# Performance work log

Hardware: AMD Instinct MI355X
Metric: run time of the kernel (lower is better)

## Reference

```python
import jax, jax.numpy as jnp
import numpy as np

S, D = 4096, 512


def setup_inputs() -> dict:
    key = jax.random.key(0)
    ks = jax.random.split(key, 10)
    names = ['x', 'w_ql', 'w_kl', 'w_qr', 'w_kr', 'w_qg', 'w_kg', 'w_qloc', 'w_kloc', 'w_v']
    shapes = [(S, D)] + [(D, D)] * 9
    scale = [1.0] + [float(np.sqrt(2.0 / (D + D)))] * 9  # xavier-ish for weights
    return {n: jax.random.normal(k, sh, dtype=jnp.float32) * s
            for n, k, sh, s in zip(names, ks, shapes, scale)}


def reference(x, w_ql, w_kl, w_qr, w_kr, w_qg, w_kg, w_qloc, w_kloc, w_v):
    # x: [S, D]
    s, d = x.shape
    norm = jnp.sqrt(jnp.asarray(d, x.dtype))
    # strict upper triangle (j > i) is masked for the left boundary,
    # strict lower triangle (i > j) for the right boundary
    mask_up = jnp.triu(jnp.ones((s, s), dtype=bool), k=1)

    ql, kl = x @ w_ql, x @ w_kl
    qr, kr = x @ w_qr, x @ w_kr

    neg_inf = jnp.asarray(-jnp.inf, x.dtype)
    left_scores = jnp.where(mask_up, neg_inf, ql @ kl.T) / norm            # [S,S]
    left_boundary = jax.nn.softmax(left_scores, axis=1)
    right_scores = jnp.where(mask_up.T, neg_inf, qr @ kr.T) / norm
    right_boundary = jax.nn.softmax(right_scores, axis=1)

    # left_boundary @ triu(ones)  == forward cumsum along columns
    # right_boundary @ tril(ones) == reverse cumsum along columns
    left_cdf = jnp.cumsum(left_boundary, axis=1)
    right_cdf = jnp.cumsum(right_boundary[:, ::-1], axis=1)[:, ::-1]
    att_mask = left_cdf * right_cdf                                        # [S,S]

    s_glb = (x @ w_qg) @ (x @ w_kg).T                                      # [S,S]
    s_loc = ((x @ w_qloc) @ (x @ w_kloc).T) * att_mask                     # additive local path
    score = (s_glb + s_loc) / norm

    att_weight = jax.nn.softmax(score, axis=1)
    att_output = att_weight @ (x @ w_v)                                    # [S,D]
    return att_output, att_weight
```

## Files before the change

### kernel.cpp

```cpp
#include <hip/hip_runtime.h>


#define SS 4096
#define DD 512
#define INV_NORM 0.04419417382415922f

typedef _Float16 f16;
typedef f16 f16x8 __attribute__((ext_vector_type(8)));
typedef f16 f16x4 __attribute__((ext_vector_type(4)));
typedef float f32x4 __attribute__((ext_vector_type(4)));
typedef unsigned short ushort;
typedef ushort ushort4v __attribute__((ext_vector_type(4)));

#define GAS __attribute__((address_space(1)))
#define LAS __attribute__((address_space(3)))

__device__ __forceinline__ void ldsdma16(const void* g, void* l) {
  __builtin_amdgcn_global_load_lds((const GAS void*)g, (LAS void*)l, 16, 0, 0);
}

__device__ __forceinline__ ushort f2bf(float f) {
  unsigned u = __float_as_uint(f);
  return (ushort)((u + 0x7FFFu + ((u >> 16) & 1u)) >> 16);
}
__device__ __forceinline__ float bf2f(ushort h) {
  return __uint_as_float((unsigned)h << 16);
}

__device__ __forceinline__ void stage16(const f16* __restrict__ src, int ldk, f16* lds, int k0) {
  const int tid  = threadIdx.x;
  const int lane = tid & 63;
  const int wv   = tid >> 6;
  const int rb   = wv * 8 + (lane >> 3);
  const int cs   = lane & 7;
#pragma unroll
  for (int c = 0; c < 4; ++c) {
    const int r = c * 32 + rb;
    const int q = cs ^ (r & 7);
    ldsdma16(src + (size_t)r * ldk + k0 + q * 8, lds + c * 2048 + wv * 512);
  }
}

__device__ __forceinline__ f16x8 fragld(const f16* lds, int r0, int qb) {
  const int lane = threadIdx.x & 63;
  const int r = r0 + (lane & 15);
  const int q = (qb + (lane >> 4)) ^ (r & 7);
  return *(const f16x8*)(lds + r * 64 + q * 8);
}

__device__ __forceinline__ void mma64(const f16* As, const f16* Bs, f32x4 acc[2][8]) {
  const int wv = threadIdx.x >> 6;
#pragma unroll
  for (int ks = 0; ks < 2; ++ks) {
    const f16x8 a0 = fragld(As, wv * 32,      ks * 4);
    const f16x8 a1 = fragld(As, wv * 32 + 16, ks * 4);
#pragma unroll
    for (int j = 0; j < 8; ++j) {
      const f16x8 b = fragld(Bs, j * 16, ks * 4);
      acc[0][j] = __builtin_amdgcn_mfma_f32_16x16x32_f16(a0, b, acc[0][j], 0, 0, 0);
      acc[1][j] = __builtin_amdgcn_mfma_f32_16x16x32_f16(a1, b, acc[1][j], 0, 0, 0);
    }
  }
}

__global__ void k_cvt_x(const float* __restrict__ x, f16* __restrict__ xh) {
  const size_t i = ((size_t)blockIdx.x * 256 + threadIdx.x) * 4;
  const float4 f = *(const float4*)(x + i);
  f16x4 h = { (f16)f.x, (f16)f.y, (f16)f.z, (f16)f.w };
  *(f16x4*)(xh + i) = h;
}

__global__ void k_trw(const float* w0, const float* w1, const float* w2, const float* w3,
                      const float* w4, const float* w5, const float* w6, const float* w7,
                      const float* w8, f16* __restrict__ wt) {
  const float* srcs[9] = {w0, w1, w2, w3, w4, w5, w6, w7, w8};
  const float* src = srcs[blockIdx.z];
  f16* dst = wt + (size_t)blockIdx.z * DD * DD;
  __shared__ float t[32][33];
  const int n0 = blockIdx.x * 32, k0 = blockIdx.y * 32;
  const int tx = threadIdx.x, ty = threadIdx.y;
#pragma unroll
  for (int i = 0; i < 32; i += 8)
    t[ty + i][tx] = src[(size_t)(k0 + ty + i) * DD + n0 + tx];
  __syncthreads();
#pragma unroll
  for (int i = 0; i < 32; i += 8)
    dst[(size_t)(n0 + ty + i) * DD + k0 + tx] = (f16)t[tx][ty + i];
}

__global__ void k_trv(const f16* __restrict__ v, f16* __restrict__ vt) {
  __shared__ f16 t[32][33];
  const int n0 = blockIdx.x * 32, s0 = blockIdx.y * 32;
  const int tx = threadIdx.x, ty = threadIdx.y;
#pragma unroll
  for (int i = 0; i < 32; i += 8)
    t[ty + i][tx] = v[(size_t)(s0 + ty + i) * DD + n0 + tx];
  __syncthreads();
#pragma unroll
  for (int i = 0; i < 32; i += 8)
    vt[(size_t)(n0 + ty + i) * SS + s0 + tx] = t[tx][ty + i];
}

__global__ __launch_bounds__(256, 3) void k_proj(const f16* __restrict__ xh,
                                                 const f16* __restrict__ wt,
                                                 f16* __restrict__ proj) {
  __shared__ __align__(16) f16 As[8192];
  __shared__ __align__(16) f16 Bs[8192];
  const int z = blockIdx.z;
  const f16* B = wt + (size_t)z * DD * DD;
  f16* C = proj + (size_t)z * SS * DD;
  const int R0 = blockIdx.y * 128, C0 = blockIdx.x * 128;
  f32x4 acc[2][8];
#pragma unroll
  for (int i = 0; i < 2; ++i)
#pragma unroll
    for (int j = 0; j < 8; ++j) acc[i][j] = (f32x4){0.f, 0.f, 0.f, 0.f};
  for (int kb = 0; kb < DD / 64; ++kb) {
    __syncthreads();
    stage16(xh + (size_t)R0 * DD, DD, As, kb * 64);
    stage16(B  + (size_t)C0 * DD, DD, Bs, kb * 64);
    __syncthreads();
    mma64(As, Bs, acc);
  }
  const int lane = threadIdx.x & 63, wv = threadIdx.x >> 6;
  const int mm = lane & 15, quad = lane >> 4;
#pragma unroll
  for (int i = 0; i < 2; ++i)
#pragma unroll
    for (int j = 0; j < 8; ++j)
#pragma unroll
      for (int r = 0; r < 4; ++r)
        C[(size_t)(R0 + wv * 32 + i * 16 + quad * 4 + r) * DD + C0 + j * 16 + mm] =
            (f16)acc[i][j][r];
}

__global__ __launch_bounds__(256, 3) void k_bnd(const f16* __restrict__ proj,
                                                f16* __restrict__ eL,
                                                f16* __restrict__ eR) {
  const int t = blockIdx.x, dir = blockIdx.y;
  int rbk = (int)((sqrtf(8.f * t + 1.f) - 1.f) * 0.5f);
  while ((rbk + 1) * (rbk + 2) / 2 <= t) ++rbk;
  while (rbk * (rbk + 1) / 2 > t) --rbk;
  int jt = t - rbk * (rbk + 1) / 2;
  if (dir) { jt = 31 - jt; rbk = 31 - rbk; }
  __shared__ __align__(16) f16 As[8192];
  __shared__ __align__(16) f16 Bs[8192];
  const f16* q  = proj + (size_t)(dir ? 2 : 0) * SS * DD;
  const f16* kp = proj + (size_t)(dir ? 3 : 1) * SS * DD;
  const int R0 = rbk * 128, C0 = jt * 128;
  f32x4 acc[2][8];
#pragma unroll
  for (int i = 0; i < 2; ++i)
#pragma unroll
    for (int j = 0; j < 8; ++j) acc[i][j] = (f32x4){0.f, 0.f, 0.f, 0.f};
  for (int kb = 0; kb < DD / 64; ++kb) {
    __syncthreads();
    stage16(q  + (size_t)R0 * DD, DD, As, kb * 64);
    stage16(kp + (size_t)C0 * DD, DD, Bs, kb * 64);
    __syncthreads();
    mma64(As, Bs, acc);
  }
  const int lane = threadIdx.x & 63, wv = threadIdx.x >> 6;
  const int mm = lane & 15, quad = lane >> 4;
  const bool diag = (jt == rbk);
  f16* outp = dir ? eR : eL;
#pragma unroll
  for (int i = 0; i < 2; ++i)
#pragma unroll
    for (int r = 0; r < 4; ++r) {
      const int rl = wv * 32 + i * 16 + quad * 4 + r;
#pragma unroll
      for (int j = 0; j < 8; ++j) {
        const int cl = j * 16 + mm;
        const float sc = acc[i][j][r] * INV_NORM;
        const bool bad = diag && (dir ? (cl < rl) : (cl > rl));
        const float e = bad ? 0.f : __expf(sc);
        outp[(size_t)(R0 + rl) * SS + (C0 + cl)] = (f16)e;
      }
    }
}

__global__ __launch_bounds__(1024) void k_cumsum(f16* __restrict__ eL,
                                                 const f16* __restrict__ eR) {
  const int i = blockIdx.x;
  const int tid = threadIdx.x, lane = tid & 63, wv = tid >> 6;
  __shared__ float wsL[16], wsR[16];
  const int j0 = tid * 4;

  float pl[4] = {0.f, 0.f, 0.f, 0.f};
  if (j0 <= i) {
    const f16x4 hl = *(const f16x4*)(eL + (size_t)i * SS + j0);
#pragma unroll
    for (int u = 0; u < 4; ++u) pl[u] = (j0 + u <= i) ? (float)hl[u] : 0.f;
  }
#pragma unroll
  for (int u = 1; u < 4; ++u) pl[u] += pl[u - 1];
  const float Tl = pl[3];
  float sl = Tl;
#pragma unroll
  for (int d = 1; d < 64; d <<= 1) {
    const float o = __shfl_up(sl, (unsigned)d, 64);
    if (lane >= d) sl += o;
  }
  if (lane == 63) wsL[wv] = sl;

  float rr[4] = {0.f, 0.f, 0.f, 0.f}, pr[4];
  if (j0 + 3 >= i) {
    const f16x4 hr = *(const f16x4*)(eR + (size_t)i * SS + j0);
#pragma unroll
    for (int u = 0; u < 4; ++u) rr[u] = (j0 + u >= i) ? (float)hr[u] : 0.f;
  }
  pr[0] = rr[0];
#pragma unroll
  for (int u = 1; u < 4; ++u) pr[u] = pr[u - 1] + rr[u];
  const float Tr = pr[3];
  float sr = Tr;
#pragma unroll
  for (int d = 1; d < 64; d <<= 1) {
    const float o = __shfl_up(sr, (unsigned)d, 64);
    if (lane >= d) sr += o;
  }
  if (lane == 63) wsR[wv] = sr;

  __syncthreads();
  float offL = 0.f, totL = 0.f, offR = 0.f, totR = 0.f;
#pragma unroll
  for (int ww = 0; ww < 16; ++ww) {
    const float a = wsL[ww], b = wsR[ww];
    if (ww < wv) { offL += a; offR += b; }
    totL += a; totR += b;
  }
  const float exL = offL + sl - Tl;
  const float exR = offR + sr - Tr;
  const float invL = 1.f / totL, invR = 1.f / totR;

  f16x4 out;
#pragma unroll
  for (int u = 0; u < 4; ++u) {
    const int j = j0 + u;
    const float cdfL = (exL + pl[u]) * invL;
    const float pre  = exR + pr[u];
    const float cdfR = (totR - pre + rr[u]) * invR;
    const float m = (j < i) ? cdfL : ((j > i) ? cdfR : 1.f);
    out[u] = (f16)m;
  }
  *(f16x4*)(eL + (size_t)i * SS + j0) = out;
}

__global__ __launch_bounds__(256, 2) void k_score(const f16* __restrict__ proj,
                                                  const f16* __restrict__ mask,
                                                  f16* __restrict__ ehalf,
                                                  float* __restrict__ lsc) {
  __shared__ __align__(16) f16 Ag[8192];
  __shared__ __align__(16) f16 Bg[8192];
  __shared__ __align__(16) f16 Al[8192];
  __shared__ __align__(16) f16 Bl[8192];
  const int jt = blockIdx.x, rbk = blockIdx.y;
  const f16* qg = proj + (size_t)4 * SS * DD;
  const f16* kg = proj + (size_t)5 * SS * DD;
  const f16* ql = proj + (size_t)6 * SS * DD;
  const f16* kl = proj + (size_t)7 * SS * DD;
  const int R0 = rbk * 128, C0 = jt * 128;
  f32x4 ag[2][8], al[2][8];
#pragma unroll
  for (int i = 0; i < 2; ++i)
#pragma unroll
    for (int j = 0; j < 8; ++j) {
      ag[i][j] = (f32x4){0.f, 0.f, 0.f, 0.f};
      al[i][j] = (f32x4){0.f, 0.f, 0.f, 0.f};
    }
  for (int kb = 0; kb < DD / 64; ++kb) {
    __syncthreads();
    stage16(qg + (size_t)R0 * DD, DD, Ag, kb * 64);
    stage16(kg + (size_t)C0 * DD, DD, Bg, kb * 64);
    stage16(ql + (size_t)R0 * DD, DD, Al, kb * 64);
    stage16(kl + (size_t)C0 * DD, DD, Bl, kb * 64);
    __syncthreads();
    mma64(Ag, Bg, ag);
    mma64(Al, Bl, al);
  }
  const int lane = threadIdx.x & 63, wv = threadIdx.x >> 6;
  const int mm = lane & 15, quad = lane >> 4;
  float ls[2][4];
#pragma unroll
  for (int i = 0; i < 2; ++i)
#pragma unroll
    for (int r = 0; r < 4; ++r) ls[i][r] = 0.f;
#pragma unroll
  for (int i = 0; i < 2; ++i)
#pragma unroll
    for (int r = 0; r < 4; ++r) {
      const int rg = R0 + wv * 32 + i * 16 + quad * 4 + r;
#pragma unroll
      for (int j = 0; j < 8; ++j) {
        const int cg = C0 + j * 16 + mm;
        const float mk = (float)mask[(size_t)rg * SS + cg];
        const float scv = (ag[i][j][r] + al[i][j][r] * mk) * INV_NORM;
        const float e = __expf(scv);
        ehalf[(size_t)rg * SS + cg] = (f16)e;
        ls[i][r] += e;
      }
    }
#pragma unroll
  for (int d = 1; d < 16; d <<= 1)
#pragma unroll
    for (int i = 0; i < 2; ++i)
#pragma unroll
      for (int r = 0; r < 4; ++r)
        ls[i][r] += __shfl_xor(ls[i][r], d, 64);
  if (mm == 0) {
#pragma unroll
    for (int i = 0; i < 2; ++i)
#pragma unroll
      for (int r = 0; r < 4; ++r)
        atomicAdd(&lsc[R0 + wv * 32 + i * 16 + quad * 4 + r], ls[i][r]);
  }
}

__global__ __launch_bounds__(256, 4) void k_pv(const f16* __restrict__ ehalf,
                                               const f16* __restrict__ vt,
                                               ushort* __restrict__ part) {
  __shared__ __align__(16) f16 As[8192];
  __shared__ __align__(16) f16 Bs[8192];
  const int C0 = blockIdx.x * 128, R0 = blockIdx.y * 128, zk = blockIdx.z;
  f32x4 acc[2][8];
#pragma unroll
  for (int i = 0; i < 2; ++i)
#pragma unroll
    for (int j = 0; j < 8; ++j) acc[i][j] = (f32x4){0.f, 0.f, 0.f, 0.f};
  for (int kb = 0; kb < 16; ++kb) {
    const int k0 = zk * 1024 + kb * 64;
    __syncthreads();
    stage16(ehalf + (size_t)R0 * SS, SS, As, k0);
    stage16(vt    + (size_t)C0 * SS, SS, Bs, k0);
    __syncthreads();
    mma64(As, Bs, acc);
  }
  const int lane = threadIdx.x & 63, wv = threadIdx.x >> 6;
  const int mm = lane & 15, quad = lane >> 4;
  ushort* P = part + (size_t)zk * SS * DD;
#pragma unroll
  for (int i = 0; i < 2; ++i)
#pragma unroll
    for (int j = 0; j < 8; ++j)
#pragma unroll
      for (int r = 0; r < 4; ++r)
        P[(size_t)(R0 + wv * 32 + i * 16 + quad * 4 + r) * DD + C0 + j * 16 + mm] =
            f2bf(acc[i][j][r]);
}

__global__ void k_fin(const f16* __restrict__ ehalf, const ushort* __restrict__ part,
                      const float* __restrict__ lsc, float* __restrict__ outw,
                      float* __restrict__ O) {
  const int bx = blockIdx.x;
  if (bx < 8192) {
    const size_t idx = ((size_t)bx * 256 + threadIdx.x) * 8;
    const int row = (int)(idx >> 12);
    const float inv = 1.f / lsc[row];
    const f16x8 h = *(const f16x8*)(ehalf + idx);
    float4 a = { (float)h[0] * inv, (float)h[1] * inv, (float)h[2] * inv, (float)h[3] * inv };
    float4 b = { (float)h[4] * inv, (float)h[5] * inv, (float)h[6] * inv, (float)h[7] * inv };
    *(float4*)(outw + idx) = a;
    *(float4*)(outw + idx + 4) = b;
  } else {
    const size_t idx = ((size_t)(bx - 8192) * 256 + threadIdx.x) * 4;
    const int row = (int)(idx >> 9);
    float s0 = 0.f, s1 = 0.f, s2 = 0.f, s3 = 0.f;
#pragma unroll
    for (int p = 0; p < 4; ++p) {
      const ushort4v v = *(const ushort4v*)(part + (size_t)p * SS * DD + idx);
      s0 += bf2f(v[0]); s1 += bf2f(v[1]); s2 += bf2f(v[2]); s3 += bf2f(v[3]);
    }
    const float inv = 1.f / lsc[row];
    float4 s = { s0 * inv, s1 * inv, s2 * inv, s3 * inv };
    *(float4*)(O + idx) = s;
  }
}

extern "C" void kernel_launch(void* const* d_in, const int* in_sizes, int n_in,
                              void* d_out, int out_size, void* d_ws, size_t ws_size,
                              hipStream_t stream) {
  (void)in_sizes; (void)n_in; (void)out_size; (void)ws_size;
  const float* x = (const float*)d_in[0];
  const float* w[9];
  for (int i = 0; i < 9; ++i) w[i] = (const float*)d_in[1 + i];
  float* O    = (float*)d_out;
  float* outw = O + (size_t)SS * DD;

  char* ws = (char*)d_ws;
  size_t off = 0;
  auto alloc = [&](size_t b) { void* p = ws + off; off += (b + 255) & ~(size_t)255; return p; };
  f16* xh     = (f16*)alloc((size_t)SS * DD * 2);
  f16* wt     = (f16*)alloc((size_t)9 * DD * DD * 2);
  f16* proj   = (f16*)alloc((size_t)9 * SS * DD * 2);
  f16* vt     = (f16*)alloc((size_t)DD * SS * 2);
  f16* eL     = (f16*)alloc((size_t)SS * SS * 2);
  f16* eR     = (f16*)alloc((size_t)SS * SS * 2);
  f16* ehalf  = (f16*)alloc((size_t)SS * SS * 2);
  float* lsc  = (float*)alloc((size_t)SS * 4);
  ushort* part = (ushort*)eR;

  hipMemsetAsync(lsc, 0, (size_t)SS * 4, stream);
  k_cvt_x<<<SS * DD / 1024, 256, 0, stream>>>(x, xh);
  k_trw<<<dim3(16, 16, 9), dim3(32, 8), 0, stream>>>(w[0], w[1], w[2], w[3], w[4],
                                                     w[5], w[6], w[7], w[8], wt);
  k_proj<<<dim3(4, 32, 9), 256, 0, stream>>>(xh, wt, proj);
  k_trv<<<dim3(16, 128), dim3(32, 8), 0, stream>>>(proj + (size_t)8 * SS * DD, vt);
  k_bnd<<<dim3(528, 2), 256, 0, stream>>>(proj, eL, eR);
  k_cumsum<<<SS, 1024, 0, stream>>>(eL, eR);
  k_score<<<dim3(32, 32), 256, 0, stream>>>(proj, eL, ehalf, lsc);
  k_pv<<<dim3(4, 32, 4), 256, 0, stream>>>(ehalf, vt, part);
  k_fin<<<10240, 256, 0, stream>>>(ehalf, part, lsc, outw, O);
}
```

Measured before the change: 293.3 us.

## Stage GEMM epilogues through swizzled LDS for coalesced 16-byte stores; fuse small launches

The output tiles of the projection, boundary, score and PV GEMMs are first written into an XOR-swizzled LDS buffer. Each block then writes them to global memory as coalesced 16-byte vectors, replacing scattered 2-byte stores. The score kernel also loads its mask tile into LDS with vector loads. The x conversion is folded into the weight-transpose launch, and the lsc memset moves into k_cumsum, which removes two launches. The cost is extra barriers and LDS traffic in every epilogue.

```diff
diff --git a/kernel.cpp b/kernel.cpp
--- a/kernel.cpp
+++ b/kernel.cpp
@@ -10,7 +10,6 @@
 typedef f16 f16x4 __attribute__((ext_vector_type(4)));
 typedef float f32x4 __attribute__((ext_vector_type(4)));
 typedef unsigned short ushort;
-typedef ushort ushort4v __attribute__((ext_vector_type(4)));
 
 #define GAS __attribute__((address_space(1)))
 #define LAS __attribute__((address_space(3)))
@@ -25,6 +24,10 @@
 }
 __device__ __forceinline__ float bf2f(ushort h) {
   return __uint_as_float((unsigned)h << 16);
+}
+
+__device__ __forceinline__ int eswz(int r, int c) {
+  return r * 128 + (c ^ (((r >> 2) & 3) << 4));
 }
 
 __device__ __forceinline__ void stage16(const f16* __restrict__ src, int ldk, f16* lds, int k0) {
@@ -63,19 +66,37 @@
   }
 }
 
-__global__ void k_cvt_x(const float* __restrict__ x, f16* __restrict__ xh) {
-  const size_t i = ((size_t)blockIdx.x * 256 + threadIdx.x) * 4;
-  const float4 f = *(const float4*)(x + i);
-  f16x4 h = { (f16)f.x, (f16)f.y, (f16)f.z, (f16)f.w };
-  *(f16x4*)(xh + i) = h;
+__device__ __forceinline__ void tile_out(const f16* T, f16* __restrict__ dst,
+                                         int R0, int C0, int ld) {
+#pragma unroll
+  for (int it = 0; it < 8; ++it) {
+    const int o = it * 256 + threadIdx.x;
+    const int rr = o >> 4, c8 = (o & 15) * 8;
+    const f16x8 v = *(const f16x8*)&T[eswz(rr, c8)];
+    *(f16x8*)(dst + (size_t)(R0 + rr) * ld + C0 + c8) = v;
+  }
 }
 
 __global__ void k_trw(const float* w0, const float* w1, const float* w2, const float* w3,
                       const float* w4, const float* w5, const float* w6, const float* w7,
-                      const float* w8, f16* __restrict__ wt) {
+                      const float* w8, const float* __restrict__ x,
+                      f16* __restrict__ wt, f16* __restrict__ xh) {
+  const int z = blockIdx.z;
+  if (z == 9) {
+    const int b = blockIdx.y * 16 + blockIdx.x;
+    const int t = b * 256 + (threadIdx.y * 32 + threadIdx.x);
+    const size_t base = (size_t)t * 32;
+#pragma unroll
+    for (int u = 0; u < 8; ++u) {
+      const float4 f = *(const float4*)(x + base + u * 4);
+      f16x4 h = { (f16)f.x, (f16)f.y, (f16)f.z, (f16)f.w };
+      *(f16x4*)(xh + base + u * 4) = h;
+    }
+    return;
+  }
   const float* srcs[9] = {w0, w1, w2, w3, w4, w5, w6, w7, w8};
-  const float* src = srcs[blockIdx.z];
-  f16* dst = wt + (size_t)blockIdx.z * DD * DD;
+  const float* src = srcs[z];
+  f16* dst = wt + (size_t)z * DD * DD;
   __shared__ float t[32][33];
   const int n0 = blockIdx.x * 32, k0 = blockIdx.y * 32;
   const int tx = threadIdx.x, ty = threadIdx.y;
@@ -104,8 +125,9 @@
 __global__ __launch_bounds__(256, 3) void k_proj(const f16* __restrict__ xh,
                                                  const f16* __restrict__ wt,
                                                  f16* __restrict__ proj) {
-  __shared__ __align__(16) f16 As[8192];
-  __shared__ __align__(16) f16 Bs[8192];
+  __shared__ __align__(16) f16 SH[16384];
+  f16* As = SH;
+  f16* Bs = SH + 8192;
   const int z = blockIdx.z;
   const f16* B = wt + (size_t)z * DD * DD;
   f16* C = proj + (size_t)z * SS * DD;
@@ -124,14 +146,16 @@
   }
   const int lane = threadIdx.x & 63, wv = threadIdx.x >> 6;
   const int mm = lane & 15, quad = lane >> 4;
+  __syncthreads();
 #pragma unroll
   for (int i = 0; i < 2; ++i)
 #pragma unroll
     for (int j = 0; j < 8; ++j)
 #pragma unroll
       for (int r = 0; r < 4; ++r)
-        C[(size_t)(R0 + wv * 32 + i * 16 + quad * 4 + r) * DD + C0 + j * 16 + mm] =
-            (f16)acc[i][j][r];
+        SH[eswz(wv * 32 + i * 16 + quad * 4 + r, j * 16 + mm)] = (f16)acc[i][j][r];
+  __syncthreads();
+  tile_out(SH, C, R0, C0, DD);
 }
 
 __global__ __launch_bounds__(256, 3) void k_bnd(const f16* __restrict__ proj,
@@ -143,8 +167,9 @@
   while (rbk * (rbk + 1) / 2 > t) --rbk;
   int jt = t - rbk * (rbk + 1) / 2;
   if (dir) { jt = 31 - jt; rbk = 31 - rbk; }
-  __shared__ __align__(16) f16 As[8192];
-  __shared__ __align__(16) f16 Bs[8192];
+  __shared__ __align__(16) f16 SH[16384];
+  f16* As = SH;
+  f16* Bs = SH + 8192;
   const f16* q  = proj + (size_t)(dir ? 2 : 0) * SS * DD;
   const f16* kp = proj + (size_t)(dir ? 3 : 1) * SS * DD;
   const int R0 = rbk * 128, C0 = jt * 128;
@@ -163,7 +188,7 @@
   const int lane = threadIdx.x & 63, wv = threadIdx.x >> 6;
   const int mm = lane & 15, quad = lane >> 4;
   const bool diag = (jt == rbk);
-  f16* outp = dir ? eR : eL;
+  __syncthreads();
 #pragma unroll
   for (int i = 0; i < 2; ++i)
 #pragma unroll
@@ -174,17 +199,20 @@
         const int cl = j * 16 + mm;
         const float sc = acc[i][j][r] * INV_NORM;
         const bool bad = diag && (dir ? (cl < rl) : (cl > rl));
-        const float e = bad ? 0.f : __expf(sc);
-        outp[(size_t)(R0 + rl) * SS + (C0 + cl)] = (f16)e;
+        SH[eswz(rl, cl)] = (f16)(bad ? 0.f : __expf(sc));
       }
     }
+  __syncthreads();
+  tile_out(SH, dir ? eR : eL, R0, C0, SS);
 }
 
 __global__ __launch_bounds__(1024) void k_cumsum(f16* __restrict__ eL,
-                                                 const f16* __restrict__ eR) {
+                                                 const f16* __restrict__ eR,
+                                                 float* __restrict__ lsc) {
   const int i = blockIdx.x;
   const int tid = threadIdx.x, lane = tid & 63, wv = tid >> 6;
   __shared__ float wsL[16], wsR[16];
+  if (tid == 0) lsc[i] = 0.f;
   const int j0 = tid * 4;
 
   float pl[4] = {0.f, 0.f, 0.f, 0.f};
@@ -251,10 +279,11 @@
                                                   const f16* __restrict__ mask,
                                                   f16* __restrict__ ehalf,
                                                   float* __restrict__ lsc) {
-  __shared__ __align__(16) f16 Ag[8192];
-  __shared__ __align__(16) f16 Bg[8192];
-  __shared__ __align__(16) f16 Al[8192];
-  __shared__ __align__(16) f16 Bl[8192];
+  __shared__ __align__(16) f16 SH[32768];
+  f16* Ag = SH;
+  f16* Bg = SH + 8192;
+  f16* Al = SH + 16384;
+  f16* Bl = SH + 24576;
   const int jt = blockIdx.x, rbk = blockIdx.y;
   const f16* qg = proj + (size_t)4 * SS * DD;
   const f16* kg = proj + (size_t)5 * SS * DD;
@@ -281,6 +310,16 @@
   }
   const int lane = threadIdx.x & 63, wv = threadIdx.x >> 6;
   const int mm = lane & 15, quad = lane >> 4;
+  __syncthreads();
+#pragma unroll
+  for (int it = 0; it < 8; ++it) {
+    const int o = it * 256 + threadIdx.x;
+    const int rr = o >> 4, c8 = (o & 15) * 8;
+    const f16x8 m = *(const f16x8*)(mask + (size_t)(R0 + rr) * SS + C0 + c8);
+    *(f16x8*)&SH[eswz(rr, c8)] = m;
+  }
+  __syncthreads();
+  f16* TE = SH + 16384;
   float ls[2][4];
 #pragma unroll
   for (int i = 0; i < 2; ++i)
@@ -290,14 +329,14 @@
   for (int i = 0; i < 2; ++i)
 #pragma unroll
     for (int r = 0; r < 4; ++r) {
-      const int rg = R0 + wv * 32 + i * 16 + quad * 4 + r;
+      const int rl = wv * 32 + i * 16 + quad * 4 + r;
 #pragma unroll
       for (int j = 0; j < 8; ++j) {
-        const int cg = C0 + j * 16 + mm;
-        const float mk = (float)mask[(size_t)rg * SS + cg];
+        const int cl = j * 16 + mm;
+        const float mk = (float)SH[eswz(rl, cl)];
         const float scv = (ag[i][j][r] + al[i][j][r] * mk) * INV_NORM;
         const float e = __expf(scv);
-        ehalf[(size_t)rg * SS + cg] = (f16)e;
+        TE[eswz(rl, cl)] = (f16)e;
         ls[i][r] += e;
       }
     }
@@ -315,13 +354,16 @@
       for (int r = 0; r < 4; ++r)
         atomicAdd(&lsc[R0 + wv * 32 + i * 16 + quad * 4 + r], ls[i][r]);
   }
+  __syncthreads();
+  tile_out(TE, ehalf, R0, C0, SS);
 }
 
 __global__ __launch_bounds__(256, 4) void k_pv(const f16* __restrict__ ehalf,
                                                const f16* __restrict__ vt,
                                                ushort* __restrict__ part) {
-  __shared__ __align__(16) f16 As[8192];
-  __shared__ __align__(16) f16 Bs[8192];
+  __shared__ __align__(16) f16 SH[16384];
+  f16* As = SH;
+  f16* Bs = SH + 8192;
   const int C0 = blockIdx.x * 128, R0 = blockIdx.y * 128, zk = blockIdx.z;
   f32x4 acc[2][8];
 #pragma unroll
@@ -338,15 +380,17 @@
   }
   const int lane = threadIdx.x & 63, wv = threadIdx.x >> 6;
   const int mm = lane & 15, quad = lane >> 4;
-  ushort* P = part + (size_t)zk * SS * DD;
+  ushort* TU = (ushort*)SH;
+  __syncthreads();
 #pragma unroll
   for (int i = 0; i < 2; ++i)
 #pragma unroll
     for (int j = 0; j < 8; ++j)
 #pragma unroll
       for (int r = 0; r < 4; ++r)
-        P[(size_t)(R0 + wv * 32 + i * 16 + quad * 4 + r) * DD + C0 + j * 16 + mm] =
-            f2bf(acc[i][j][r]);
+        TU[eswz(wv * 32 + i * 16 + quad * 4 + r, j * 16 + mm)] = f2bf(acc[i][j][r]);
+  __syncthreads();
+  tile_out(SH, (f16*)(part + (size_t)zk * SS * DD), R0, C0, DD);
 }
 
 __global__ void k_fin(const f16* __restrict__ ehalf, const ushort* __restrict__ part,
@@ -366,6 +410,7 @@
     const size_t idx = ((size_t)(bx - 8192) * 256 + threadIdx.x) * 4;
     const int row = (int)(idx >> 9);
     float s0 = 0.f, s1 = 0.f, s2 = 0.f, s3 = 0.f;
+    typedef ushort ushort4v __attribute__((ext_vector_type(4)));
 #pragma unroll
     for (int p = 0; p < 4; ++p) {
       const ushort4v v = *(const ushort4v*)(part + (size_t)p * SS * DD + idx);
@@ -400,14 +445,12 @@
   float* lsc  = (float*)alloc((size_t)SS * 4);
   ushort* part = (ushort*)eR;
 
-  hipMemsetAsync(lsc, 0, (size_t)SS * 4, stream);
-  k_cvt_x<<<SS * DD / 1024, 256, 0, stream>>>(x, xh);
-  k_trw<<<dim3(16, 16, 9), dim3(32, 8), 0, stream>>>(w[0], w[1], w[2], w[3], w[4],
-                                                     w[5], w[6], w[7], w[8], wt);
+  k_trw<<<dim3(16, 16, 10), dim3(32, 8), 0, stream>>>(w[0], w[1], w[2], w[3], w[4],
+                                                      w[5], w[6], w[7], w[8], x, wt, xh);
   k_proj<<<dim3(4, 32, 9), 256, 0, stream>>>(xh, wt, proj);
   k_trv<<<dim3(16, 128), dim3(32, 8), 0, stream>>>(proj + (size_t)8 * SS * DD, vt);
   k_bnd<<<dim3(528, 2), 256, 0, stream>>>(proj, eL, eR);
-  k_cumsum<<<SS, 1024, 0, stream>>>(eL, eR);
+  k_cumsum<<<SS, 1024, 0, stream>>>(eL, eR, lsc);
   k_score<<<dim3(32, 32), 256, 0, stream>>>(proj, eL, ehalf, lsc);
   k_pv<<<dim3(4, 32, 4), 256, 0, stream>>>(ehalf, vt, part);
   k_fin<<<10240, 256, 0, stream>>>(ehalf, part, lsc, outw, O);
```

Result: no change. 296.3 us (+1.0%).
